# Optimization experiments

Hardware: AMD Instinct MI355X
Metric: run time of the kernel (lower is better)

The kernel has to match this reference:

```python
import jax, jax.numpy as jnp
import numpy as np

N_NODES = 100000


def gcn_conv(x, edge_index, W, b, n_nodes):
    """PyG GCNConv: h = x @ W; add self-loops; symmetric deg norm; sum-aggregate; + bias."""
    src, dst = edge_index[0], edge_index[1]
    loop = jnp.arange(n_nodes, dtype=src.dtype)
    src = jnp.concatenate([src, loop])  # [E + N]
    dst = jnp.concatenate([dst, loop])
    w = jnp.ones(src.shape[0], dtype=x.dtype)  # edge_weight=None -> ones
    deg = jax.ops.segment_sum(w, dst, num_segments=n_nodes)  # in-degree incl. self-loop
    dinv = jnp.where(deg > 0, jax.lax.rsqrt(deg), 0.0).astype(x.dtype)
    norm = dinv[src] * w * dinv[dst]  # [E + N]
    h = x @ W  # [N, d_out] transform first (PyG order)
    msgs = norm[:, None] * h[src]  # [E + N, d_out] gathered, normalized messages
    out = jax.ops.segment_sum(msgs, dst, num_segments=n_nodes)
    return out + b


def setup_inputs() -> dict:
    key = jax.random.key(0)
    k1, k2, k3, k4 = jax.random.split(key, 4)
    d_in, d_hid, d_out = 128, 128, 64
    E = 3200000
    x = jax.random.normal(k1, (N_NODES, d_in), dtype=jnp.float32)
    edge_index = jax.random.randint(k2, (2, E), 0, N_NODES, dtype=jnp.int64)
    W1 = jax.random.normal(k3, (d_in, d_hid), dtype=jnp.float32) / np.sqrt(d_in)
    b1 = jnp.zeros((d_hid,), dtype=jnp.float32)
    W2 = jax.random.normal(k4, (d_hid, d_out), dtype=jnp.float32) / np.sqrt(d_hid)
    b2 = jnp.zeros((d_out,), dtype=jnp.float32)
    return {"x": x, "edge_index": edge_index, "W1": W1, "b1": b1, "W2": W2, "b2": b2}


def reference(x, edge_index, W1, b1, W2, b2):
    h = gcn_conv(x, edge_index, W1, b1, N_NODES)
    h = jax.nn.relu(h)
    out = gcn_conv(h, edge_index, W2, b2, N_NODES)
    return out
```

## Files before the change

kernel.cpp:

```cpp
#include <hip/hip_runtime.h>


#define N_NODES 100000
#define NBLK2 256
#define NBUCK2 782
#define NCH 13
#define NKEY (NBUCK2 * NCH)

#define QS   8192.0f
#define IQS  1.220703125e-4f

typedef __attribute__((ext_vector_type(8))) short short8;
typedef __attribute__((ext_vector_type(4))) float f32x4;

__device__ __forceinline__ unsigned short f2bf(float f) {
    union { float f; unsigned u; } c; c.f = f;
    unsigned r = (c.u + 0x7fffu + ((c.u >> 16) & 1u)) >> 16;
    return (unsigned short)r;
}
__device__ __forceinline__ unsigned packbf(float a, float b) {
    return (unsigned)f2bf(a) | ((unsigned)f2bf(b) << 16);
}
__device__ __forceinline__ unsigned short q13(float v) {
    int i = __float2int_rn(v * QS);
    i = i < -32767 ? -32767 : (i > 32767 ? 32767 : i);
    return (unsigned short)(i & 0xffff);
}

__global__ void detect64_k(const unsigned long long* __restrict__ ei, int* __restrict__ flag) {
    unsigned long long v = ei[threadIdx.x & 63];
    unsigned long long bad = __ballot(v >= (1ULL << 32));
    if (threadIdx.x == 0) *flag = (bad == 0ULL) ? 1 : 0;
}

__device__ __forceinline__ int edge_at(const void* ei, int is64, long long idx) {
    if (is64) return (int)((const long long*)ei)[idx];
    return ((const int*)ei)[idx];
}

__global__ __launch_bounds__(256) void count1_k(const void* __restrict__ ei,
                                                const int* __restrict__ flag,
                                                int* __restrict__ bhist, int E) {
    __shared__ int lh[NKEY];
    int t = threadIdx.x;
    for (int i = t; i < NKEY; i += 256) lh[i] = 0;
    __syncthreads();
    int is64 = *flag;
    int C = (E + NBLK2 - 1) / NBLK2;
    int lo = blockIdx.x * C;
    int hi = lo + C; if (hi > E) hi = E;
    for (int e = lo + t; e < hi; e += 256) {
        int s = edge_at(ei, is64, e);
        int d = edge_at(ei, is64, (long long)E + e);
        if ((unsigned)d >= (unsigned)N_NODES) continue;
        if ((unsigned)s >= (unsigned)N_NODES) s = 0;
        atomicAdd(&lh[(d >> 7) * NCH + (s >> 13)], 1);
    }
    __syncthreads();
    int* dst = bhist + (size_t)blockIdx.x * NKEY;
    for (int i = t; i < NKEY; i += 256) dst[i] = lh[i];
}

__global__ void colsum_k(const int* __restrict__ bhist, int* __restrict__ colsum) {
    int k = blockIdx.x * 256 + threadIdx.x;
    if (k >= NKEY) return;
    int s = 0;
#pragma unroll 4
    for (int b = 0; b < NBLK2; ++b) s += bhist[(size_t)b * NKEY + k];
    colsum[k] = s;
}

__global__ void scan1_k(const int* __restrict__ cnt, int* __restrict__ partial,
                        int* __restrict__ bsum, int n) {
    __shared__ int sm[256];
    int t = threadIdx.x;
    int base = blockIdx.x * 1024 + t * 4;
    int v[4]; int loc = 0;
#pragma unroll
    for (int j = 0; j < 4; ++j) { v[j] = (base + j < n) ? cnt[base + j] : 0; loc += v[j]; }
    sm[t] = loc; __syncthreads();
    for (int off = 1; off < 256; off <<= 1) {
        int x = (t >= off) ? sm[t - off] : 0;
        __syncthreads();
        sm[t] += x;
        __syncthreads();
    }
    int incl = sm[t];
    int run = incl - loc;
    if (t == 255) bsum[blockIdx.x] = incl;
#pragma unroll
    for (int j = 0; j < 4; ++j) {
        if (base + j < n) partial[base + j] = run;
        run += v[j];
    }
}

__global__ void scan2_k(int* __restrict__ bsum, int nb) {
    __shared__ int sm[256];
    int t = threadIdx.x;
    int v[16]; int loc = 0;
#pragma unroll
    for (int i = 0; i < 16; ++i) {
        int idx = t * 16 + i;
        v[i] = (idx < nb) ? bsum[idx] : 0;
        loc += v[i];
    }
    sm[t] = loc; __syncthreads();
    for (int off = 1; off < 256; off <<= 1) {
        int x = (t >= off) ? sm[t - off] : 0;
        __syncthreads();
        sm[t] += x;
        __syncthreads();
    }
    int run = sm[t] - loc;
#pragma unroll
    for (int i = 0; i < 16; ++i) {
        int idx = t * 16 + i;
        if (idx < nb) bsum[idx] = run;
        run += v[i];
    }
}

__global__ void scanadd_k(const int* __restrict__ bsum, int* __restrict__ arr,
                          const int* __restrict__ raw, int* __restrict__ tot, int n) {
    int base = blockIdx.x * 1024 + threadIdx.x * 4;
    int add = bsum[blockIdx.x];
#pragma unroll
    for (int j = 0; j < 4; ++j) {
        int i = base + j;
        if (i < n) {
            int v = arr[i] + add;
            arr[i] = v;
            if (i == n - 1) *tot = v + raw[i];
        }
    }
}

__global__ void colprefix_k(const int* __restrict__ bhist, const int* __restrict__ keybase,
                            int* __restrict__ bbase) {
    int k = blockIdx.x * 256 + threadIdx.x;
    if (k >= NKEY) return;
    int run = keybase[k];
#pragma unroll 8
    for (int b = 0; b < NBLK2; ++b) {
        size_t i = (size_t)b * NKEY + k;
        int c = bhist[i];
        bbase[i] = run;
        run += c;
    }
}

__global__ void dinv_k(const int* __restrict__ cnt, float* __restrict__ dinv, int n) {
    int i = blockIdx.x * 256 + threadIdx.x;
    if (i < n) dinv[i] = rsqrtf((float)(cnt[i] + 1));
}

__global__ __launch_bounds__(256) void write1_k(const void* __restrict__ ei,
                                                const int* __restrict__ flag,
                                                const int* __restrict__ bbase,
                                                unsigned* __restrict__ pairs, int E) {
    __shared__ int lofs[NKEY];
    int t = threadIdx.x;
    const int* src0 = bbase + (size_t)blockIdx.x * NKEY;
    for (int i = t; i < NKEY; i += 256) lofs[i] = src0[i];
    __syncthreads();
    int is64 = *flag;
    int C = (E + NBLK2 - 1) / NBLK2;
    int lo = blockIdx.x * C;
    int hi = lo + C; if (hi > E) hi = E;
    for (int e = lo + t; e < hi; e += 256) {
        int s = edge_at(ei, is64, e);
        int d = edge_at(ei, is64, (long long)E + e);
        if ((unsigned)d >= (unsigned)N_NODES) continue;
        if ((unsigned)s >= (unsigned)N_NODES) s = 0;
        int key = (d >> 7) * NCH + (s >> 13);
        int p = atomicAdd(&lofs[key], 1);
        pairs[p] = (unsigned)s | ((unsigned)(d & 127) << 17);
    }
}

__global__ __launch_bounds__(256) void degree_k(const unsigned* __restrict__ pairs,
                                                const int* __restrict__ keybase,
                                                const int* __restrict__ tot,
                                                int* __restrict__ cnt, int Nn) {
    __shared__ int lh[128];
    int b = blockIdx.x;
    int t = threadIdx.x;
    if (t < 128) lh[t] = 0;
    __syncthreads();
    int lo = keybase[b * NCH];
    int hi = (b == NBUCK2 - 1) ? *tot : keybase[(b + 1) * NCH];
    for (int i = lo + t; i < hi; i += 256) {
        unsigned p = __builtin_nontemporal_load(pairs + i);
        atomicAdd(&lh[p >> 17], 1);
    }
    __syncthreads();
    int n0 = b << 7;
    if (t < 128 && n0 + t < Nn) cnt[n0 + t] = lh[t];
}

__global__ void prep_w_k(const float* __restrict__ W1, const float* __restrict__ W2,
                         unsigned short* __restrict__ w1bf, unsigned short* __restrict__ w2bf) {
    int i = blockIdx.x * 256 + threadIdx.x;
    if (i < 128 * 128) { int k = i >> 7, f = i & 127; w1bf[f * 128 + k] = f2bf(W1[i]); }
    if (i < 128 * 64)  { int k = i >> 6, f = i & 63;  w2bf[f * 128 + k] = f2bf(W2[i]); }
}

__global__ __launch_bounds__(256) void gemm1_k(const float* __restrict__ x,
                                               const unsigned short* __restrict__ w1bf,
                                               const float* __restrict__ dinv,
                                               unsigned* __restrict__ h1, int Nn) {
    __shared__ __align__(16) unsigned short sA[128][136];
    __shared__ __align__(16) unsigned short sB[64][136];
    int tid = threadIdx.x;
    int n0g = blockIdx.x * 64;
    {
        const uint4* src = (const uint4*)w1bf;
#pragma unroll
        for (int l = 0; l < 8; ++l) {
            int idx = tid + l * 256;
            int f = idx >> 4, kq = idx & 15;
            *(uint4*)&sA[f][kq * 8] = src[idx];
        }
    }
    {
        int n = tid >> 2, kq = tid & 3;
        int gn = n0g + n; if (gn >= Nn) gn = Nn - 1;
        const float4* xr = (const float4*)(x + (size_t)gn * 128 + kq * 32);
        unsigned short* dst = &sB[n][kq * 32];
#pragma unroll
        for (int i = 0; i < 8; ++i) {
            float4 v = xr[i];
            dst[i * 4 + 0] = f2bf(v.x); dst[i * 4 + 1] = f2bf(v.y);
            dst[i * 4 + 2] = f2bf(v.z); dst[i * 4 + 3] = f2bf(v.w);
        }
    }
    __syncthreads();
    int wave = tid >> 6, lane = tid & 63;
    int quad = lane >> 4, l16 = lane & 15;
    f32x4 z = {0.f, 0.f, 0.f, 0.f};
    f32x4 acc[8];
#pragma unroll
    for (int t = 0; t < 8; ++t) acc[t] = z;
#pragma unroll
    for (int kk = 0; kk < 4; ++kk) {
        int kb = kk * 32 + quad * 8;
        short8 a = *(const short8*)&sB[wave * 16 + l16][kb];
#pragma unroll
        for (int ft = 0; ft < 8; ++ft) {
            short8 b = *(const short8*)&sA[ft * 16 + l16][kb];
            acc[ft] = __builtin_amdgcn_mfma_f32_16x16x32_bf16(a, b, acc[ft], 0, 0, 0);
        }
    }
    float dv[4];
#pragma unroll
    for (int r = 0; r < 4; ++r) {
        int gn = n0g + wave * 16 + quad * 4 + r;
        if (gn >= Nn) gn = Nn - 1;
        dv[r] = dinv[gn];
    }
    __syncthreads();
    unsigned short (*sC)[136] = sA;
#pragma unroll
    for (int ft = 0; ft < 8; ++ft)
#pragma unroll
        for (int r = 0; r < 4; ++r)
            sC[wave * 16 + quad * 4 + r][ft * 16 + l16] = q13(dv[r] * acc[ft][r]);
    __syncthreads();
#pragma unroll
    for (int l = 0; l < 4; ++l) {
        int idx = tid + l * 256;
        int row = idx >> 4, g = idx & 15;
        int gn = n0g + row;
        if (gn < Nn) {
            ushort4 A = *(ushort4*)&sC[row][g * 4];
            ushort4 B = *(ushort4*)&sC[row][g * 4 + 64];
            uint4 o;
            o.x = (unsigned)A.x | ((unsigned)B.x << 16);
            o.y = (unsigned)A.y | ((unsigned)B.y << 16);
            o.z = (unsigned)A.z | ((unsigned)B.z << 16);
            o.w = (unsigned)A.w | ((unsigned)B.w << 16);
            *(uint4*)&h1[(size_t)gn * 64 + g * 4] = o;
        }
    }
}

__global__ __launch_bounds__(256) void gemm2_k(const unsigned* __restrict__ hr,
                                               const unsigned short* __restrict__ w2bf,
                                               const float* __restrict__ dinv,
                                               unsigned* __restrict__ h2, int Nn) {
    __shared__ __align__(16) unsigned short sA[64][136];
    __shared__ __align__(16) unsigned short sB[64][136];
    int tid = threadIdx.x;
    int n0g = blockIdx.x * 64;
    {
        const uint4* src = (const uint4*)w2bf;
#pragma unroll
        for (int l = 0; l < 4; ++l) {
            int idx = tid + l * 256;
            int f = idx >> 4, kq = idx & 15;
            *(uint4*)&sA[f][kq * 8] = src[idx];
        }
    }
    {
        const uint4* src = (const uint4*)hr;
#pragma unroll
        for (int l = 0; l < 4; ++l) {
            int idx = tid + l * 256;
            int row = idx >> 4, q = idx & 15;
            int gn = n0g + row; if (gn >= Nn) gn = Nn - 1;
            *(uint4*)&sB[row][q * 8] = src[(size_t)gn * 16 + q];
        }
    }
    __syncthreads();
    int wave = tid >> 6, lane = tid & 63;
    int quad = lane >> 4, l16 = lane & 15;
    f32x4 z = {0.f, 0.f, 0.f, 0.f};
    f32x4 acc[4];
#pragma unroll
    for (int t = 0; t < 4; ++t) acc[t] = z;
#pragma unroll
    for (int kk = 0; kk < 4; ++kk) {
        int kb = kk * 32 + quad * 8;
        short8 a = *(const short8*)&sB[wave * 16 + l16][kb];
#pragma unroll
        for (int ft = 0; ft < 4; ++ft) {
            short8 b = *(const short8*)&sA[ft * 16 + l16][kb];
            acc[ft] = __builtin_amdgcn_mfma_f32_16x16x32_bf16(a, b, acc[ft], 0, 0, 0);
        }
    }
    float dv[4];
#pragma unroll
    for (int r = 0; r < 4; ++r) {
        int gn = n0g + wave * 16 + quad * 4 + r;
        if (gn >= Nn) gn = Nn - 1;
        dv[r] = dinv[gn];
    }
    __syncthreads();
    unsigned short (*sC)[136] = sA;
#pragma unroll
    for (int ft = 0; ft < 4; ++ft)
#pragma unroll
        for (int r = 0; r < 4; ++r)
            sC[wave * 16 + quad * 4 + r][ft * 16 + l16] = q13(dv[r] * acc[ft][r]);
    __syncthreads();
#pragma unroll
    for (int l = 0; l < 2; ++l) {
        int idx = tid + l * 256;
        int row = idx >> 3, g = idx & 7;
        int gn = n0g + row;
        if (gn < Nn) {
            ushort4 A = *(ushort4*)&sC[row][g * 4];
            ushort4 B = *(ushort4*)&sC[row][g * 4 + 32];
            uint4 o;
            o.x = (unsigned)A.x | ((unsigned)B.x << 16);
            o.y = (unsigned)A.y | ((unsigned)B.y << 16);
            o.z = (unsigned)A.z | ((unsigned)B.z << 16);
            o.w = (unsigned)A.w | ((unsigned)B.w << 16);
            *(uint4*)&h2[(size_t)gn * 32 + g * 4] = o;
        }
    }
}

__global__ __launch_bounds__(1024) void agg1_k(const unsigned* __restrict__ h,
                                               const unsigned* __restrict__ pairs,
                                               const int* __restrict__ keybase,
                                               const int* __restrict__ tot,
                                               const float* __restrict__ dinv,
                                               const float* __restrict__ bias,
                                               unsigned* __restrict__ out, int Nn) {
    extern __shared__ int iacc[];
    int tid = threadIdx.x, lane = tid & 63, wave = tid >> 6;
    int b = blockIdx.x, n0 = b << 7;
    for (int i = tid; i < 128 * 64; i += 1024) {
        int row = i >> 6, q = i & 63;
        unsigned u = (n0 + row < Nn) ? h[(size_t)(n0 + row) * 64 + q] : 0u;
        iacc[row * 128 + q] = (int)(short)(u & 0xffffu);
        iacc[row * 128 + 64 + q] = ((int)u) >> 16;
    }
    __syncthreads();
    int lo = keybase[b * NCH];
    int hi = (b == NBUCK2 - 1) ? *tot : keybase[(b + 1) * NCH];
    for (int base = lo + wave * 64; base < hi; base += 1024) {
        int idx = base + lane;
        unsigned pv = pairs[(idx < hi) ? idx : (hi - 1)];
        int m = hi - base; if (m > 64) m = 64;
        int j = 0;
        for (; j + 4 <= m; j += 4) {
            unsigned p0 = __shfl(pv, j),     p1 = __shfl(pv, j + 1);
            unsigned p2 = __shfl(pv, j + 2), p3 = __shfl(pv, j + 3);
            unsigned u0 = h[((p0 & 0x1FFFFu) << 6) + lane];
            unsigned u1 = h[((p1 & 0x1FFFFu) << 6) + lane];
            unsigned u2 = h[((p2 & 0x1FFFFu) << 6) + lane];
            unsigned u3 = h[((p3 & 0x1FFFFu) << 6) + lane];
            int* a0 = &iacc[((p0 >> 17) << 7) + lane];
            atomicAdd(a0, (int)(short)(u0 & 0xffffu)); atomicAdd(a0 + 64, ((int)u0) >> 16);
            int* a1 = &iacc[((p1 >> 17) << 7) + lane];
            atomicAdd(a1, (int)(short)(u1 & 0xffffu)); atomicAdd(a1 + 64, ((int)u1) >> 16);
            int* a2 = &iacc[((p2 >> 17) << 7) + lane];
            atomicAdd(a2, (int)(short)(u2 & 0xffffu)); atomicAdd(a2 + 64, ((int)u2) >> 16);
            int* a3 = &iacc[((p3 >> 17) << 7) + lane];
            atomicAdd(a3, (int)(short)(u3 & 0xffffu)); atomicAdd(a3 + 64, ((int)u3) >> 16);
        }
        for (; j < m; ++j) {
            unsigned p = __shfl(pv, j);
            unsigned u = h[((p & 0x1FFFFu) << 6) + lane];
            int* a = &iacc[((p >> 17) << 7) + lane];
            atomicAdd(a, (int)(short)(u & 0xffffu)); atomicAdd(a + 64, ((int)u) >> 16);
        }
    }
    __syncthreads();
    int nn = Nn - n0; if (nn > 128) nn = 128;
    for (int i = tid; i < nn * 64; i += 1024) {
        int row = i >> 6, q = i & 63;
        float di = dinv[n0 + row];
        float sx = (float)iacc[row * 128 + 2 * q] * IQS;
        float sy = (float)iacc[row * 128 + 2 * q + 1] * IQS;
        float r0 = fmaxf(fmaf(di, sx, bias[2 * q]), 0.f);
        float r1 = fmaxf(fmaf(di, sy, bias[2 * q + 1]), 0.f);
        out[(size_t)(n0 + row) * 64 + q] = packbf(r0, r1);
    }
}

__global__ __launch_bounds__(1024) void agg2_k(const unsigned* __restrict__ h,
                                               const unsigned* __restrict__ pairs,
                                               const int* __restrict__ keybase,
                                               const int* __restrict__ tot,
                                               const float* __restrict__ dinv,
                                               const float* __restrict__ bias,
                                               float* __restrict__ out, int Nn) {
    __shared__ int iacc[128 * 64];
    int tid = threadIdx.x, lane = tid & 63, wave = tid >> 6;
    int half = lane >> 5, fl = lane & 31;
    int b = blockIdx.x, n0 = b << 7;
    for (int i = tid; i < 128 * 32; i += 1024) {
        int row = i >> 5, q = i & 31;
        unsigned u = (n0 + row < Nn) ? h[(size_t)(n0 + row) * 32 + q] : 0u;
        iacc[row * 64 + q] = (int)(short)(u & 0xffffu);
        iacc[row * 64 + 32 + q] = ((int)u) >> 16;
    }
    __syncthreads();
    int lo = keybase[b * NCH];
    int hi = (b == NBUCK2 - 1) ? *tot : keybase[(b + 1) * NCH];
    for (int base = lo + wave * 64; base < hi; base += 1024) {
        int idx = base + lane;
        unsigned pv = pairs[(idx < hi) ? idx : (hi - 1)];
        int m = hi - base; if (m > 64) m = 64;
        int j = 0;
        for (; j + 8 <= m; j += 8) {
            unsigned p0 = __shfl(pv, j + half);
            unsigned p1 = __shfl(pv, j + 2 + half);
            unsigned p2 = __shfl(pv, j + 4 + half);
            unsigned p3 = __shfl(pv, j + 6 + half);
            unsigned u0 = h[((p0 & 0x1FFFFu) << 5) + fl];
            unsigned u1 = h[((p1 & 0x1FFFFu) << 5) + fl];
            unsigned u2 = h[((p2 & 0x1FFFFu) << 5) + fl];
            unsigned u3 = h[((p3 & 0x1FFFFu) << 5) + fl];
            int* a0 = &iacc[((p0 >> 17) << 6) + fl];
            atomicAdd(a0, (int)(short)(u0 & 0xffffu)); atomicAdd(a0 + 32, ((int)u0) >> 16);
            int* a1 = &iacc[((p1 >> 17) << 6) + fl];
            atomicAdd(a1, (int)(short)(u1 & 0xffffu)); atomicAdd(a1 + 32, ((int)u1) >> 16);
            int* a2 = &iacc[((p2 >> 17) << 6) + fl];
            atomicAdd(a2, (int)(short)(u2 & 0xffffu)); atomicAdd(a2 + 32, ((int)u2) >> 16);
            int* a3 = &iacc[((p3 >> 17) << 6) + fl];
            atomicAdd(a3, (int)(short)(u3 & 0xffffu)); atomicAdd(a3 + 32, ((int)u3) >> 16);
        }
        for (; j < m; j += 2) {
            int q = j + half;
            unsigned p = __shfl(pv, (q < m) ? q : j);
            if (q < m) {
                unsigned u = h[((p & 0x1FFFFu) << 5) + fl];
                int* a = &iacc[((p >> 17) << 6) + fl];
                atomicAdd(a, (int)(short)(u & 0xffffu)); atomicAdd(a + 32, ((int)u) >> 16);
            }
        }
    }
    __syncthreads();
    int nn = Nn - n0; if (nn > 128) nn = 128;
    for (int i = tid; i < nn * 64; i += 1024) {
        int row = i >> 6, f = i & 63;
        float di = dinv[n0 + row];
        float s = (float)iacc[row * 64 + f] * IQS;
        out[(size_t)(n0 + row) * 64 + f] = fmaf(di, s, bias[f]);
    }
}

extern "C" void kernel_launch(void* const* d_in, const int* in_sizes, int n_in,
                              void* d_out, int out_size, void* d_ws, size_t ws_size,
                              hipStream_t stream) {
    const float* x  = (const float*)d_in[0];
    const void*  ei = d_in[1];
    const float* W1 = (const float*)d_in[2];
    const float* b1 = (const float*)d_in[3];
    const float* W2 = (const float*)d_in[4];
    const float* b2 = (const float*)d_in[5];

    const int N = N_NODES;
    const int E = in_sizes[1] / 2;

    char* w = (char*)d_ws;
    size_t off = 0;
    auto take = [&](size_t bytes) {
        void* p = w + off;
        off = (off + bytes + 255) & ~(size_t)255;
        return p;
    };
    int*   flag    = (int*)take(2 * sizeof(int));
    int*   tot     = flag + 1;
    int*   cnt     = (int*)take((size_t)N * 4);
    int*   bsumB   = (int*)take(4096 * 4);
    int*   colsum  = (int*)take((size_t)NKEY * 4);
    int*   keybase = (int*)take((size_t)NKEY * 4);
    float* dinv    = (float*)take((size_t)N * 4);
    unsigned* pairs = (unsigned*)take((size_t)E * 4);
    unsigned short* w1bf = (unsigned short*)take(128 * 128 * 2);
    unsigned short* w2bf = (unsigned short*)take(64 * 128 * 2);
    unsigned* hr   = (unsigned*)take((size_t)N * 64 * 4);
    unsigned* h2   = (unsigned*)take((size_t)N * 32 * 4);
    (void)ws_size; (void)n_in; (void)out_size;

    int* bhist = (int*)hr;
    int* bbase = (int*)h2;

    unsigned* h1 = (unsigned*)d_out;

    const int nscanK = (NKEY + 1023) / 1024;
    const int ngridK = (NKEY + 255) / 256;

    detect64_k<<<1, 64, 0, stream>>>((const unsigned long long*)ei, flag);
    count1_k<<<NBLK2, 256, 0, stream>>>(ei, flag, bhist, E);
    colsum_k<<<ngridK, 256, 0, stream>>>(bhist, colsum);
    scan1_k<<<nscanK, 256, 0, stream>>>(colsum, keybase, bsumB, NKEY);
    scan2_k<<<1, 256, 0, stream>>>(bsumB, nscanK);
    scanadd_k<<<nscanK, 256, 0, stream>>>(bsumB, keybase, colsum, tot, NKEY);
    colprefix_k<<<ngridK, 256, 0, stream>>>(bhist, keybase, bbase);
    write1_k<<<NBLK2, 256, 0, stream>>>(ei, flag, bbase, pairs, E);
    degree_k<<<NBUCK2, 256, 0, stream>>>(pairs, keybase, tot, cnt, N);
    dinv_k<<<(N + 255) / 256, 256, 0, stream>>>(cnt, dinv, N);
    prep_w_k<<<64, 256, 0, stream>>>(W1, W2, w1bf, w2bf);

    gemm1_k<<<(N + 63) / 64, 256, 0, stream>>>(x, w1bf, dinv, h1, N);
    agg1_k<<<NBUCK2, 1024, 128 * 128 * 4, stream>>>(h1, pairs, keybase, tot, dinv, b1, hr, N);
    gemm2_k<<<(N + 63) / 64, 256, 0, stream>>>(hr, w2bf, dinv, h2, N);
    agg2_k<<<NBUCK2, 1024, 0, stream>>>(h2, pairs, keybase, tot, dinv, b2, (float*)d_out, N);
}
```

Measured before the change: 441.1 us.

## Pack two biased 16-bit features into one 64-bit LDS atomic in aggregation

Quantized features are now stored with a +32768 offset so two unsigned lanes can be packed into a 64-bit word and accumulated with a single 64-bit LDS atomicAdd, halving the number of shared-memory atomics. Gathers switch from 32-bit per lane to 16-byte uint4 loads, with several edges handled per wave at once. The bias is removed afterwards using the per-node add count (degree plus one). This relies on the 32-bit halves not overflowing and on cnt matching the number of additions exactly.

Result: slower. 464.5 us (+5.3%).

```diff
diff --git a/kernel.cpp b/kernel.cpp
--- a/kernel.cpp
+++ b/kernel.cpp
@@ -21,10 +21,13 @@
 __device__ __forceinline__ unsigned packbf(float a, float b) {
     return (unsigned)f2bf(a) | ((unsigned)f2bf(b) << 16);
 }
-__device__ __forceinline__ unsigned short q13(float v) {
+__device__ __forceinline__ unsigned short q13b(float v) {
     int i = __float2int_rn(v * QS);
     i = i < -32767 ? -32767 : (i > 32767 ? 32767 : i);
-    return (unsigned short)(i & 0xffff);
+    return (unsigned short)(i + 32768);
+}
+__device__ __forceinline__ unsigned long long pk64(unsigned w) {
+    return ((unsigned long long)(w >> 16) << 32) | (unsigned long long)(w & 0xffffu);
 }
 
 __global__ void detect64_k(const unsigned long long* __restrict__ ei, int* __restrict__ flag) {
@@ -265,7 +268,7 @@
     for (int ft = 0; ft < 8; ++ft)
 #pragma unroll
         for (int r = 0; r < 4; ++r)
-            sC[wave * 16 + quad * 4 + r][ft * 16 + l16] = q13(dv[r] * acc[ft][r]);
+            sC[wave * 16 + quad * 4 + r][ft * 16 + l16] = q13b(dv[r] * acc[ft][r]);
     __syncthreads();
 #pragma unroll
     for (int l = 0; l < 4; ++l) {
@@ -342,7 +345,7 @@
     for (int ft = 0; ft < 4; ++ft)
 #pragma unroll
         for (int r = 0; r < 4; ++r)
-            sC[wave * 16 + quad * 4 + r][ft * 16 + l16] = q13(dv[r] * acc[ft][r]);
+            sC[wave * 16 + quad * 4 + r][ft * 16 + l16] = q13b(dv[r] * acc[ft][r]);
     __syncthreads();
 #pragma unroll
     for (int l = 0; l < 2; ++l) {
@@ -366,17 +369,19 @@
                                                const unsigned* __restrict__ pairs,
                                                const int* __restrict__ keybase,
                                                const int* __restrict__ tot,
+                                               const int* __restrict__ cnt,
                                                const float* __restrict__ dinv,
                                                const float* __restrict__ bias,
                                                unsigned* __restrict__ out, int Nn) {
-    extern __shared__ int iacc[];
+    extern __shared__ unsigned long long acc2[];
     int tid = threadIdx.x, lane = tid & 63, wave = tid >> 6;
+    int qtr = lane >> 4, fq = lane & 15;
     int b = blockIdx.x, n0 = b << 7;
+    const uint4* hq = (const uint4*)h;
     for (int i = tid; i < 128 * 64; i += 1024) {
         int row = i >> 6, q = i & 63;
         unsigned u = (n0 + row < Nn) ? h[(size_t)(n0 + row) * 64 + q] : 0u;
-        iacc[row * 128 + q] = (int)(short)(u & 0xffffu);
-        iacc[row * 128 + 64 + q] = ((int)u) >> 16;
+        acc2[row * 64 + q] = pk64(u);
     }
     __syncthreads();
     int lo = keybase[b * NCH];
@@ -386,27 +391,38 @@
         unsigned pv = pairs[(idx < hi) ? idx : (hi - 1)];
         int m = hi - base; if (m > 64) m = 64;
         int j = 0;
+        for (; j + 16 <= m; j += 16) {
+#pragma unroll
+            for (int k = 0; k < 4; ++k) {
+                unsigned p = __shfl(pv, j + 4 * k + qtr);
+                uint4 u = hq[((p & 0x1FFFFu) << 4) + fq];
+                unsigned long long* a = &acc2[((p >> 17) << 6) + 4 * fq];
+                atomicAdd(a + 0, pk64(u.x));
+                atomicAdd(a + 1, pk64(u.y));
+                atomicAdd(a + 2, pk64(u.z));
+                atomicAdd(a + 3, pk64(u.w));
+            }
+        }
         for (; j + 4 <= m; j += 4) {
-            unsigned p0 = __shfl(pv, j),     p1 = __shfl(pv, j + 1);
-            unsigned p2 = __shfl(pv, j + 2), p3 = __shfl(pv, j + 3);
-            unsigned u0 = h[((p0 & 0x1FFFFu) << 6) + lane];
-            unsigned u1 = h[((p1 & 0x1FFFFu) << 6) + lane];
-            unsigned u2 = h[((p2 & 0x1FFFFu) << 6) + lane];
-            unsigned u3 = h[((p3 & 0x1FFFFu) << 6) + lane];
-            int* a0 = &iacc[((p0 >> 17) << 7) + lane];
-            atomicAdd(a0, (int)(short)(u0 & 0xffffu)); atomicAdd(a0 + 64, ((int)u0) >> 16);
-            int* a1 = &iacc[((p1 >> 17) << 7) + lane];
-            atomicAdd(a1, (int)(short)(u1 & 0xffffu)); atomicAdd(a1 + 64, ((int)u1) >> 16);
-            int* a2 = &iacc[((p2 >> 17) << 7) + lane];
-            atomicAdd(a2, (int)(short)(u2 & 0xffffu)); atomicAdd(a2 + 64, ((int)u2) >> 16);
-            int* a3 = &iacc[((p3 >> 17) << 7) + lane];
-            atomicAdd(a3, (int)(short)(u3 & 0xffffu)); atomicAdd(a3 + 64, ((int)u3) >> 16);
-        }
-        for (; j < m; ++j) {
-            unsigned p = __shfl(pv, j);
-            unsigned u = h[((p & 0x1FFFFu) << 6) + lane];
-            int* a = &iacc[((p >> 17) << 7) + lane];
-            atomicAdd(a, (int)(short)(u & 0xffffu)); atomicAdd(a + 64, ((int)u) >> 16);
+            unsigned p = __shfl(pv, j + qtr);
+            uint4 u = hq[((p & 0x1FFFFu) << 4) + fq];
+            unsigned long long* a = &acc2[((p >> 17) << 6) + 4 * fq];
+            atomicAdd(a + 0, pk64(u.x));
+            atomicAdd(a + 1, pk64(u.y));
+            atomicAdd(a + 2, pk64(u.z));
+            atomicAdd(a + 3, pk64(u.w));
+        }
+        if (j < m) {
+            int q = j + qtr;
+            unsigned p = __shfl(pv, (q < m) ? q : j);
+            if (q < m) {
+                uint4 u = hq[((p & 0x1FFFFu) << 4) + fq];
+                unsigned long long* a = &acc2[((p >> 17) << 6) + 4 * fq];
+                atomicAdd(a + 0, pk64(u.x));
+                atomicAdd(a + 1, pk64(u.y));
+                atomicAdd(a + 2, pk64(u.z));
+                atomicAdd(a + 3, pk64(u.w));
+            }
         }
     }
     __syncthreads();
@@ -414,10 +430,15 @@
     for (int i = tid; i < nn * 64; i += 1024) {
         int row = i >> 6, q = i & 63;
         float di = dinv[n0 + row];
-        float sx = (float)iacc[row * 128 + 2 * q] * IQS;
-        float sy = (float)iacc[row * 128 + 2 * q + 1] * IQS;
-        float r0 = fmaxf(fmaf(di, sx, bias[2 * q]), 0.f);
-        float r1 = fmaxf(fmaf(di, sy, bias[2 * q + 1]), 0.f);
+        int nadds = cnt[n0 + row] + 1;
+        float deb = (float)nadds * 32768.0f;
+        int f0 = 2 * q, f1 = 2 * q + 1;
+        unsigned long long v0 = acc2[row * 64 + (f0 & 63)];
+        unsigned long long v1 = acc2[row * 64 + (f1 & 63)];
+        float s0 = ((float)(unsigned)((f0 < 64) ? (v0 & 0xffffffffu) : (v0 >> 32)) - deb) * IQS;
+        float s1 = ((float)(unsigned)((f1 < 64) ? (v1 & 0xffffffffu) : (v1 >> 32)) - deb) * IQS;
+        float r0 = fmaxf(fmaf(di, s0, bias[f0]), 0.f);
+        float r1 = fmaxf(fmaf(di, s1, bias[f1]), 0.f);
         out[(size_t)(n0 + row) * 64 + q] = packbf(r0, r1);
     }
 }
@@ -426,18 +447,19 @@
                                                const unsigned* __restrict__ pairs,
                                                const int* __restrict__ keybase,
                                                const int* __restrict__ tot,
+                                               const int* __restrict__ cnt,
                                                const float* __restrict__ dinv,
                                                const float* __restrict__ bias,
                                                float* __restrict__ out, int Nn) {
-    __shared__ int iacc[128 * 64];
+    __shared__ unsigned long long acc2[128 * 32];
     int tid = threadIdx.x, lane = tid & 63, wave = tid >> 6;
-    int half = lane >> 5, fl = lane & 31;
+    int oct = lane >> 3, fo = lane & 7;
     int b = blockIdx.x, n0 = b << 7;
+    const uint4* hq = (const uint4*)h;
     for (int i = tid; i < 128 * 32; i += 1024) {
         int row = i >> 5, q = i & 31;
         unsigned u = (n0 + row < Nn) ? h[(size_t)(n0 + row) * 32 + q] : 0u;
-        iacc[row * 64 + q] = (int)(short)(u & 0xffffu);
-        iacc[row * 64 + 32 + q] = ((int)u) >> 16;
+        acc2[row * 32 + q] = pk64(u);
     }
     __syncthreads();
     int lo = keybase[b * NCH];
@@ -447,31 +469,37 @@
         unsigned pv = pairs[(idx < hi) ? idx : (hi - 1)];
         int m = hi - base; if (m > 64) m = 64;
         int j = 0;
+        for (; j + 16 <= m; j += 16) {
+#pragma unroll
+            for (int k = 0; k < 2; ++k) {
+                unsigned p = __shfl(pv, j + 8 * k + oct);
+                uint4 u = hq[((p & 0x1FFFFu) << 3) + fo];
+                unsigned long long* a = &acc2[((p >> 17) << 5) + 4 * fo];
+                atomicAdd(a + 0, pk64(u.x));
+                atomicAdd(a + 1, pk64(u.y));
+                atomicAdd(a + 2, pk64(u.z));
+                atomicAdd(a + 3, pk64(u.w));
+            }
+        }
         for (; j + 8 <= m; j += 8) {
-            unsigned p0 = __shfl(pv, j + half);
-            unsigned p1 = __shfl(pv, j + 2 + half);
-            unsigned p2 = __shfl(pv, j + 4 + half);
-            unsigned p3 = __shfl(pv, j + 6 + half);
-            unsigned u0 = h[((p0 & 0x1FFFFu) << 5) + fl];
-            unsigned u1 = h[((p1 & 0x1FFFFu) << 5) + fl];
-            unsigned u2 = h[((p2 & 0x1FFFFu) << 5) + fl];
-            unsigned u3 = h[((p3 & 0x1FFFFu) << 5) + fl];
-            int* a0 = &iacc[((p0 >> 17) << 6) + fl];
-            atomicAdd(a0, (int)(short)(u0 & 0xffffu)); atomicAdd(a0 + 32, ((int)u0) >> 16);
-            int* a1 = &iacc[((p1 >> 17) << 6) + fl];
-            atomicAdd(a1, (int)(short)(u1 & 0xffffu)); atomicAdd(a1 + 32, ((int)u1) >> 16);
-            int* a2 = &iacc[((p2 >> 17) << 6) + fl];
-            atomicAdd(a2, (int)(short)(u2 & 0xffffu)); atomicAdd(a2 + 32, ((int)u2) >> 16);
-            int* a3 = &iacc[((p3 >> 17) << 6) + fl];
-            atomicAdd(a3, (int)(short)(u3 & 0xffffu)); atomicAdd(a3 + 32, ((int)u3) >> 16);
-        }
-        for (; j < m; j += 2) {
-            int q = j + half;
+            unsigned p = __shfl(pv, j + oct);
+            uint4 u = hq[((p & 0x1FFFFu) << 3) + fo];
+            unsigned long long* a = &acc2[((p >> 17) << 5) + 4 * fo];
+            atomicAdd(a + 0, pk64(u.x));
+            atomicAdd(a + 1, pk64(u.y));
+            atomicAdd(a + 2, pk64(u.z));
+            atomicAdd(a + 3, pk64(u.w));
+        }
+        if (j < m) {
+            int q = j + oct;
             unsigned p = __shfl(pv, (q < m) ? q : j);
             if (q < m) {
-                unsigned u = h[((p & 0x1FFFFu) << 5) + fl];
-                int* a = &iacc[((p >> 17) << 6) + fl];
-                atomicAdd(a, (int)(short)(u & 0xffffu)); atomicAdd(a + 32, ((int)u) >> 16);
+                uint4 u = hq[((p & 0x1FFFFu) << 3) + fo];
+                unsigned long long* a = &acc2[((p >> 17) << 5) + 4 * fo];
+                atomicAdd(a + 0, pk64(u.x));
+                atomicAdd(a + 1, pk64(u.y));
+                atomicAdd(a + 2, pk64(u.z));
+                atomicAdd(a + 3, pk64(u.w));
             }
         }
     }
@@ -480,7 +508,10 @@
     for (int i = tid; i < nn * 64; i += 1024) {
         int row = i >> 6, f = i & 63;
         float di = dinv[n0 + row];
-        float s = (float)iacc[row * 64 + f] * IQS;
+        int nadds = cnt[n0 + row] + 1;
+        float deb = (float)nadds * 32768.0f;
+        unsigned long long v = acc2[row * 32 + (f & 31)];
+        float s = ((float)(unsigned)((f < 32) ? (v & 0xffffffffu) : (v >> 32)) - deb) * IQS;
         out[(size_t)(n0 + row) * 64 + f] = fmaf(di, s, bias[f]);
     }
 }
@@ -540,7 +571,7 @@
     prep_w_k<<<64, 256, 0, stream>>>(W1, W2, w1bf, w2bf);
 
     gemm1_k<<<(N + 63) / 64, 256, 0, stream>>>(x, w1bf, dinv, h1, N);
-    agg1_k<<<NBUCK2, 1024, 128 * 128 * 4, stream>>>(h1, pairs, keybase, tot, dinv, b1, hr, N);
+    agg1_k<<<NBUCK2, 1024, 128 * 64 * 8, stream>>>(h1, pairs, keybase, tot, cnt, dinv, b1, hr, N);
     gemm2_k<<<(N + 63) / 64, 256, 0, stream>>>(hr, w2bf, dinv, h2, N);
-    agg2_k<<<NBUCK2, 1024, 0, stream>>>(h2, pairs, keybase, tot, dinv, b2, (float*)d_out, N);
-}
+    agg2_k<<<NBUCK2, 1024, 0, stream>>>(h2, pairs, keybase, tot, cnt, dinv, b2, (float*)d_out, N);
+}
```
